# Performance work log

Measured on AMD Instinct MI355X. Metric: run time of the kernel, lower is better.

The kernel has to match this reference:

```python
import jax, jax.numpy as jnp
import numpy as np

N = 50000      # nodes
E = 1600000    # edges (avg degree 32)
D = 128        # node_feat_size
G = 128        # graph_feat_size (must equal D for BatchNorm1d to match MLP out)
EPS = 1e-5
NEG_SLOPE = 0.01  # LeakyReLU default


def setup_inputs() -> dict:
    key = jax.random.key(0)
    ks = jax.random.split(key, 10)
    p = lambda k, sh: jax.random.normal(k, sh, dtype=jnp.float32) * 0.05
    return {
        "node_feats": jax.random.normal(ks[0], (N, D), dtype=jnp.float32),
        "src": jax.random.randint(ks[1], (E,), 0, N, dtype=jnp.int32),
        "dst": jax.random.randint(ks[2], (E,), 0, N, dtype=jnp.int32),
        # project_edge: Linear(2D -> 1); split weight into dst/src halves
        "we_dst": p(ks[3], (D,)),
        "we_src": p(ks[4], (D,)),
        "be": jnp.zeros((), jnp.float32),
        # project_node: Linear(D -> G)
        "w_proj": p(ks[5], (D, G)),
        "b_proj": jnp.zeros((G,), jnp.float32),
        # MPL: Linear(G+D -> D), ReLU, Linear(D -> D)
        "w1": p(ks[6], (G + D, D)),
        "b1": jnp.zeros((D,), jnp.float32),
        "w2": p(ks[7], (D, D)),
        "b2": jnp.zeros((D,), jnp.float32),
        # BatchNorm1d(G) affine params (training-mode batch stats)
        "gamma": jnp.ones((G,), jnp.float32),
        "beta": jnp.zeros((G,), jnp.float32),
    }


def reference(node_feats, src, dst, we_dst, we_src, be, w_proj, b_proj,
              w1, b1, w2, b2, gamma, beta):
    # Edge logits: LeakyReLU(Linear(cat([dst_feat, src_feat])))
    # Linear over a concat == sum of two per-node projections -> avoid [E, 2D] tensor.
    ld = node_feats @ we_dst            # [N]
    ls = node_feats @ we_src            # [N]
    logit = ld[dst] + ls[src] + be      # [E]
    logit = jnp.where(logit >= 0, logit, NEG_SLOPE * logit)

    # edge_softmax: softmax over incoming edges of each destination node
    m = jax.ops.segment_max(logit, dst, num_segments=N)          # [N]
    ev = jnp.exp(logit - m[dst])                                  # [E]
    denom = jax.ops.segment_sum(ev, dst, num_segments=N)         # [N]
    a = ev / denom[dst]                                           # [E]

    # src_mul_edge + sum aggregation
    hv = node_feats @ w_proj + b_proj                             # [N, G]
    msg = hv[src] * a[:, None]                                    # [E, G]
    c = jax.ops.segment_sum(msg, dst, num_segments=N)             # [N, G]
    context = jax.nn.elu(c)

    # MPL: Linear -> ReLU -> Linear, then outer ReLU (dropout is identity in eval)
    h = jnp.concatenate([context, node_feats], axis=1)            # [N, G+D]
    h = jax.nn.relu(h @ w1 + b1)
    h = h @ w2 + b2
    h = jax.nn.relu(h)

    # BatchNorm1d in training mode: biased batch statistics
    mean = jnp.mean(h, axis=0)
    var = jnp.mean((h - mean) ** 2, axis=0)
    return gamma * (h - mean) / jnp.sqrt(var + EPS) + beta
```

## Files before the change

### kernel.cpp

```cpp
#include <hip/hip_runtime.h>
#include <math.h>

#define NN 50000
#define EE 1600000
#define DD 128
#define NB 98
#define SLAB 18432
#define MROWS 32
#define MGRID 1563

typedef __attribute__((ext_vector_type(8))) short short8v;
typedef __attribute__((ext_vector_type(4))) float f32x4;
typedef __attribute__((ext_vector_type(2))) float floatx2;

#define HVB_OFF     0
#define CTXB_OFF    6400000
#define BIN_OFF     19200000
#define SRCS_OFF    26425344
#define LD_OFF      30038016
#define LS_OFF      30238016
#define START_OFF   30438016
#define CNTN_OFF    30638016
#define W1T_OFF     30838016
#define W2T_OFF     30903552
#define WPT_OFF     30936320
#define BKC_OFF     30969088
#define MEAN_OFF    30969600
#define ISTD_OFF    30970112
#define PBN_OFF     30971648
#define PBQ_OFF     31771904
#define ZERO_OFF    BKC_OFF
#define ZERO_LEN    512

__device__ __forceinline__ unsigned short f2bf(float f) {
  union { float f; unsigned u; } v; v.f = f;
  unsigned r = v.u + 0x7FFFu + ((v.u >> 16) & 1u);
  return (unsigned short)(r >> 16);
}

__global__ __launch_bounds__(256) void k_prep_w(const float* __restrict__ w1,
    const float* __restrict__ w2, const float* __restrict__ wp,
    unsigned short* __restrict__ w1t, unsigned short* __restrict__ w2t,
    unsigned short* __restrict__ wpt) {
  int t = blockIdx.x * 256 + threadIdx.x;
  if (t < 32768) {
    int n = t & 127, k = t >> 7;
    w1t[n * 256 + k] = f2bf(w1[(size_t)k * 128 + n]);
  } else if (t < 49152) {
    int i = t - 32768; int n = i & 127, k = i >> 7;
    w2t[n * 128 + k] = f2bf(w2[(size_t)k * 128 + n]);
  } else {
    int i = t - 49152; int n = i & 127, k = i >> 7;
    wpt[n * 128 + k] = f2bf(wp[(size_t)k * 128 + n]);
  }
}

__global__ __launch_bounds__(256) void k_hv2(const float* __restrict__ nf,
    const unsigned short* __restrict__ wpt, const float* __restrict__ bp,
    const float* __restrict__ wed, const float* __restrict__ wes,
    float* __restrict__ ld, float* __restrict__ ls,
    unsigned char* __restrict__ hvb) {
  __shared__ unsigned short xs[64][136];
  int tid = threadIdx.x;
  int m0 = blockIdx.x * 64;
  int c4 = tid & 31;
  float4 wdv = *(const float4*)(wed + c4 * 4);
  float4 wsv = *(const float4*)(wes + c4 * 4);
  #pragma unroll
  for (int e = 0; e < 8; ++e) {
    int idx = tid + 256 * e;
    int row = idx >> 5;
    int m = m0 + row;
    int mc = (m < NN) ? m : (NN - 1);
    float4 v = *(const float4*)(nf + (size_t)mc * 128 + c4 * 4);
    ushort4 bb;
    bb.x = f2bf(v.x); bb.y = f2bf(v.y); bb.z = f2bf(v.z); bb.w = f2bf(v.w);
    *(ushort4*)&xs[row][c4 * 4] = bb;
    float pa = v.x * wdv.x + v.y * wdv.y + v.z * wdv.z + v.w * wdv.w;
    float pb = v.x * wsv.x + v.y * wsv.y + v.z * wsv.z + v.w * wsv.w;
    #pragma unroll
    for (int o = 16; o; o >>= 1) { pa += __shfl_xor(pa, o); pb += __shfl_xor(pb, o); }
    if (c4 == 0 && m < NN) { ld[m] = pa; ls[m] = pb; }
  }
  __syncthreads();
  int wid = tid >> 6, lane = tid & 63;
  int wm = wid >> 1, wn = wid & 1;
  int l15 = lane & 15, lg = lane >> 4;
  f32x4 acc[4][2];
  #pragma unroll
  for (int nf2 = 0; nf2 < 4; ++nf2)
    #pragma unroll
    for (int mf = 0; mf < 2; ++mf) acc[nf2][mf] = (f32x4){0.f, 0.f, 0.f, 0.f};
  for (int ks = 0; ks < 4; ++ks) {
    short8v aw[4], bx[2];
    #pragma unroll
    for (int nf2 = 0; nf2 < 4; ++nf2) {
      int n = wn * 64 + nf2 * 16 + l15;
      aw[nf2] = *(const short8v*)(wpt + (size_t)n * 128 + ks * 32 + lg * 8);
    }
    #pragma unroll
    for (int mf = 0; mf < 2; ++mf)
      bx[mf] = *(const short8v*)&xs[wm * 32 + mf * 16 + l15][ks * 32 + lg * 8];
    #pragma unroll
    for (int nf2 = 0; nf2 < 4; ++nf2)
      #pragma unroll
      for (int mf = 0; mf < 2; ++mf)
        acc[nf2][mf] = __builtin_amdgcn_mfma_f32_16x16x32_bf16(aw[nf2], bx[mf], acc[nf2][mf], 0, 0, 0);
  }
  #pragma unroll
  for (int nf2 = 0; nf2 < 4; ++nf2) {
    float4 bp4 = *(const float4*)(bp + wn * 64 + nf2 * 16 + lg * 4);
    #pragma unroll
    for (int mf = 0; mf < 2; ++mf) {
      int m = m0 + wm * 32 + mf * 16 + l15;
      if (m < NN) {
        int w = __builtin_amdgcn_cvt_pk_fp8_f32(acc[nf2][mf][0] + bp4.x,
                                                acc[nf2][mf][1] + bp4.y, 0, false);
        w = __builtin_amdgcn_cvt_pk_fp8_f32(acc[nf2][mf][2] + bp4.z,
                                            acc[nf2][mf][3] + bp4.w, w, true);
        *(int*)(hvb + (size_t)m * 128 + wn * 64 + nf2 * 16 + lg * 4) = w;
      }
    }
  }
}

__global__ __launch_bounds__(256) void k_bin(const int* __restrict__ src,
    const int* __restrict__ dst, int* __restrict__ bkc,
    unsigned* __restrict__ bin) {
  __shared__ unsigned slot[8192];
  __shared__ int hist[128], sc[128], loff[128], lcur[128], gbase[128];
  int tid = threadIdx.x;
  int tbase = blockIdx.x * 8192;
  int tlen = min(8192, EE - tbase);
  unsigned pk[32];
  if (tid < 128) hist[tid] = 0;
  __syncthreads();
  #pragma unroll
  for (int k = 0; k < 32; ++k) {
    int i = k * 256 + tid;
    if (i < tlen) {
      int e = tbase + i;
      pk[k] = ((unsigned)dst[e] << 16) | (unsigned)src[e];
      atomicAdd(&hist[pk[k] >> 25], 1);
    }
  }
  __syncthreads();
  if (tid < 128) sc[tid] = hist[tid];
  __syncthreads();
  for (int off = 1; off < 128; off <<= 1) {
    int v = 0;
    if (tid < 128) v = sc[tid] + ((tid >= off) ? sc[tid - off] : 0);
    __syncthreads();
    if (tid < 128) sc[tid] = v;
    __syncthreads();
  }
  if (tid < 128) { loff[tid] = sc[tid] - hist[tid]; lcur[tid] = sc[tid] - hist[tid]; }
  __syncthreads();
  #pragma unroll
  for (int k = 0; k < 32; ++k) {
    int i = k * 256 + tid;
    if (i < tlen) {
      int r = atomicAdd(&lcur[pk[k] >> 25], 1);
      slot[r] = pk[k];
    }
  }
  __syncthreads();
  if (tid < 128) gbase[tid] = hist[tid] ? atomicAdd(&bkc[tid], hist[tid]) : 0;
  __syncthreads();
  #pragma unroll
  for (int k = 0; k < 32; ++k) {
    int i = k * 256 + tid;
    if (i < tlen) {
      unsigned p = slot[i];
      int b = p >> 25;
      bin[(size_t)b * SLAB + gbase[b] + (i - loff[b])] = p;
    }
  }
}

__global__ __launch_bounds__(256) void k_bsort(const unsigned* __restrict__ bin,
    const int* __restrict__ bkc, unsigned short* __restrict__ srcs,
    int* __restrict__ start, int* __restrict__ cntn) {
  __shared__ unsigned eL[SLAB];
  __shared__ unsigned short outL[SLAB];
  __shared__ int hist[512], scA[512], cur[512];
  int tid = threadIdx.x;
  int b = blockIdx.x;
  int base = b * SLAB;
  int cnt = bkc[b];
  int node0 = b << 9;
  int nnb = min(512, NN - node0);
  for (int i = tid; i < 512; i += 256) hist[i] = 0;
  __syncthreads();
  for (int i = tid; i < cnt; i += 256) {
    unsigned p = bin[base + i];
    eL[i] = p;
    atomicAdd(&hist[(p >> 16) & 511], 1);
  }
  __syncthreads();
  for (int i = tid; i < 512; i += 256) scA[i] = hist[i];
  __syncthreads();
  for (int off = 1; off < 512; off <<= 1) {
    int v0 = scA[tid] + ((tid >= off) ? scA[tid - off] : 0);
    int i1 = tid + 256;
    int v1 = scA[i1] + ((i1 >= off) ? scA[i1 - off] : 0);
    __syncthreads();
    scA[tid] = v0; scA[i1] = v1;
    __syncthreads();
  }
  for (int i = tid; i < 512; i += 256) {
    int ex = scA[i] - hist[i];
    cur[i] = ex;
    if (i < nnb) { start[node0 + i] = base + ex; cntn[node0 + i] = hist[i]; }
  }
  __syncthreads();
  for (int i = tid; i < cnt; i += 256) {
    unsigned p = eL[i];
    int r = atomicAdd(&cur[(p >> 16) & 511], 1);
    outL[r] = (unsigned short)(p & 0xFFFFu);
  }
  __syncthreads();
  for (int i = tid; i < cnt; i += 256) srcs[base + i] = outL[i];
}

__global__ __launch_bounds__(256) void k_agg(const unsigned char* __restrict__ hvb,
    const float* __restrict__ ld, const float* __restrict__ ls,
    const float* __restrict__ be_p, const int* __restrict__ start,
    const int* __restrict__ cntn, const unsigned short* __restrict__ srcs,
    unsigned short* __restrict__ ctxb) {
  int wid = (blockIdx.x * 256 + threadIdx.x) >> 6;
  int lane = threadIdx.x & 63;
  if (wid >= NN) return;
  int cnt = cntn[wid];
  int l8 = lane & 7, e8 = lane >> 3;
  float acc[16];
  #pragma unroll
  for (int i = 0; i < 16; ++i) acc[i] = 0.f;
  float m = -INFINITY, dsum = 0.f;
  if (cnt > 0) {
    int s = start[wid];
    float base = ld[wid] + be_p[0];
    for (int c0 = 0; c0 < cnt; c0 += 64) {
      int len = min(64, cnt - c0);
      float lg = -INFINITY;
      int sv = 0;
      if (lane < len) {
        sv = srcs[s + c0 + lane];
        float l = base + ls[sv];
        lg = (l >= 0.f) ? l : 0.01f * l;
      }
      float cm = lg;
      #pragma unroll
      for (int o = 32; o; o >>= 1) cm = fmaxf(cm, __shfl_xor(cm, o));
      float nm = fmaxf(m, cm);
      float sc = __expf(m - nm);
      #pragma unroll
      for (int i = 0; i < 16; ++i) acc[i] *= sc;
      dsum *= sc;
      float ev = (lane < len) ? __expf(lg - nm) : 0.f;
      dsum += ev;
      for (int j = 0; j < len; j += 8) {
        int jj = j + e8;
        float evj = __shfl(ev, jj);
        int svj = __shfl(sv, jj);
        if (jj < len) {
          uint4 U = *(const uint4*)(hvb + (size_t)svj * 128 + l8 * 16);
          floatx2 p;
          p = __builtin_amdgcn_cvt_pk_f32_fp8((int)U.x, false); acc[0] += evj * p[0];  acc[1] += evj * p[1];
          p = __builtin_amdgcn_cvt_pk_f32_fp8((int)U.x, true);  acc[2] += evj * p[0];  acc[3] += evj * p[1];
          p = __builtin_amdgcn_cvt_pk_f32_fp8((int)U.y, false); acc[4] += evj * p[0];  acc[5] += evj * p[1];
          p = __builtin_amdgcn_cvt_pk_f32_fp8((int)U.y, true);  acc[6] += evj * p[0];  acc[7] += evj * p[1];
          p = __builtin_amdgcn_cvt_pk_f32_fp8((int)U.z, false); acc[8] += evj * p[0];  acc[9] += evj * p[1];
          p = __builtin_amdgcn_cvt_pk_f32_fp8((int)U.z, true);  acc[10] += evj * p[0]; acc[11] += evj * p[1];
          p = __builtin_amdgcn_cvt_pk_f32_fp8((int)U.w, false); acc[12] += evj * p[0]; acc[13] += evj * p[1];
          p = __builtin_amdgcn_cvt_pk_f32_fp8((int)U.w, true);  acc[14] += evj * p[0]; acc[15] += evj * p[1];
        }
      }
      m = nm;
    }
  }
  #pragma unroll
  for (int o = 8; o <= 32; o <<= 1)
    #pragma unroll
    for (int i = 0; i < 16; ++i) acc[i] += __shfl_xor(acc[i], o);
  #pragma unroll
  for (int o = 32; o; o >>= 1) dsum += __shfl_xor(dsum, o);
  float r = (dsum > 0.f) ? (1.f / dsum) : 0.f;
  if (lane < 32) {
    int g = lane & 7, p4 = lane >> 3;
    float v0 = acc[p4 * 4 + 0] * r, v1 = acc[p4 * 4 + 1] * r;
    float v2 = acc[p4 * 4 + 2] * r, v3 = acc[p4 * 4 + 3] * r;
    v0 = (v0 > 0.f) ? v0 : expm1f(v0);
    v1 = (v1 > 0.f) ? v1 : expm1f(v1);
    v2 = (v2 > 0.f) ? v2 : expm1f(v2);
    v3 = (v3 > 0.f) ? v3 : expm1f(v3);
    uint2 u;
    u.x = (unsigned)f2bf(v0) | ((unsigned)f2bf(v1) << 16);
    u.y = (unsigned)f2bf(v2) | ((unsigned)f2bf(v3) << 16);
    *(uint2*)(ctxb + (size_t)wid * 128 + g * 16 + p4 * 4) = u;
  }
}

__global__ __launch_bounds__(256) void k_mlp2(const unsigned short* __restrict__ ctxb,
    const float* __restrict__ nf,
    const unsigned short* __restrict__ w1t, const float* __restrict__ b1,
    const unsigned short* __restrict__ w2t, const float* __restrict__ b2,
    float* __restrict__ out, float* __restrict__ pbn, float* __restrict__ pbq) {
  __shared__ unsigned short xs[MROWS][264];
  __shared__ unsigned short h1s[MROWS][136];
  __shared__ float bns[128], bnq[128];
  int tid = threadIdx.x;
  int m0 = blockIdx.x * MROWS;
  if (tid < 128) { bns[tid] = 0.f; bnq[tid] = 0.f; }
  #pragma unroll
  for (int e = 0; e < 2; ++e) {
    int idx = tid + 256 * e;
    int row = idx >> 4, c8 = idx & 15;
    int m = m0 + row; if (m >= NN) m = NN - 1;
    uint4 v = *(const uint4*)(ctxb + (size_t)m * 128 + c8 * 8);
    *(uint4*)&xs[row][c8 * 8] = v;
  }
  #pragma unroll
  for (int e = 0; e < 4; ++e) {
    int idx = tid + 256 * e;
    int row = idx >> 5, c4 = idx & 31;
    int m = m0 + row; if (m >= NN) m = NN - 1;
    float4 w = *(const float4*)(nf + (size_t)m * 128 + c4 * 4);
    ushort4 cc;
    cc.x = f2bf(w.x); cc.y = f2bf(w.y); cc.z = f2bf(w.z); cc.w = f2bf(w.w);
    *(ushort4*)&xs[row][128 + c4 * 4] = cc;
  }
  __syncthreads();
  int wid = tid >> 6, lane = tid & 63;
  int wm = wid >> 1, wn = wid & 1;
  int l15 = lane & 15, lg = lane >> 4;
  f32x4 acc[4];
  #pragma unroll
  for (int nf2 = 0; nf2 < 4; ++nf2) acc[nf2] = (f32x4){0.f, 0.f, 0.f, 0.f};
  for (int ks = 0; ks < 8; ++ks) {
    short8v a = *(const short8v*)&xs[wm * 16 + l15][ks * 32 + lg * 8];
    #pragma unroll
    for (int nf2 = 0; nf2 < 4; ++nf2) {
      int n = wn * 64 + nf2 * 16 + l15;
      short8v b = *(const short8v*)(w1t + (size_t)n * 256 + ks * 32 + lg * 8);
      acc[nf2] = __builtin_amdgcn_mfma_f32_16x16x32_bf16(a, b, acc[nf2], 0, 0, 0);
    }
  }
  {
    float b1n[4];
    #pragma unroll
    for (int nf2 = 0; nf2 < 4; ++nf2) b1n[nf2] = b1[wn * 64 + nf2 * 16 + l15];
    #pragma unroll
    for (int nf2 = 0; nf2 < 4; ++nf2)
      #pragma unroll
      for (int r = 0; r < 4; ++r) {
        int row = wm * 16 + lg * 4 + r;
        int col = wn * 64 + nf2 * 16 + l15;
        h1s[row][col] = f2bf(fmaxf(acc[nf2][r] + b1n[nf2], 0.f));
      }
  }
  __syncthreads();
  f32x4 acc2[4];
  #pragma unroll
  for (int nf2 = 0; nf2 < 4; ++nf2) acc2[nf2] = (f32x4){0.f, 0.f, 0.f, 0.f};
  for (int ks = 0; ks < 4; ++ks) {
    short8v bh = *(const short8v*)&h1s[wm * 16 + l15][ks * 32 + lg * 8];
    #pragma unroll
    for (int nf2 = 0; nf2 < 4; ++nf2) {
      int n = wn * 64 + nf2 * 16 + l15;
      short8v aw = *(const short8v*)(w2t + (size_t)n * 128 + ks * 32 + lg * 8);
      acc2[nf2] = __builtin_amdgcn_mfma_f32_16x16x32_bf16(aw, bh, acc2[nf2], 0, 0, 0);
    }
  }
  {
    int m = m0 + wm * 16 + l15;
    bool valid = (m < NN);
    float hs[4][4], hq[4][4];
    #pragma unroll
    for (int nf2 = 0; nf2 < 4; ++nf2) {
      int f0 = wn * 64 + nf2 * 16 + lg * 4;
      float4 b24 = *(const float4*)(b2 + f0);
      float h0 = fmaxf(acc2[nf2][0] + b24.x, 0.f);
      float h1v = fmaxf(acc2[nf2][1] + b24.y, 0.f);
      float h2v = fmaxf(acc2[nf2][2] + b24.z, 0.f);
      float h3v = fmaxf(acc2[nf2][3] + b24.w, 0.f);
      if (valid) {
        float4 o = make_float4(h0, h1v, h2v, h3v);
        *(float4*)(out + (size_t)m * 128 + f0) = o;
      } else { h0 = h1v = h2v = h3v = 0.f; }
      hs[nf2][0] = h0; hs[nf2][1] = h1v; hs[nf2][2] = h2v; hs[nf2][3] = h3v;
      hq[nf2][0] = h0 * h0; hq[nf2][1] = h1v * h1v;
      hq[nf2][2] = h2v * h2v; hq[nf2][3] = h3v * h3v;
    }
    #pragma unroll
    for (int o = 1; o <= 8; o <<= 1)
      #pragma unroll
      for (int nf2 = 0; nf2 < 4; ++nf2)
        #pragma unroll
        for (int r = 0; r < 4; ++r) {
          hs[nf2][r] += __shfl_xor(hs[nf2][r], o);
          hq[nf2][r] += __shfl_xor(hq[nf2][r], o);
        }
    if (l15 == 0) {
      #pragma unroll
      for (int nf2 = 0; nf2 < 4; ++nf2) {
        int f0 = wn * 64 + nf2 * 16 + lg * 4;
        #pragma unroll
        for (int r = 0; r < 4; ++r) {
          atomicAdd(&bns[f0 + r], hs[nf2][r]);
          atomicAdd(&bnq[f0 + r], hq[nf2][r]);
        }
      }
    }
  }
  __syncthreads();
  if (tid < 128) {
    pbn[(size_t)blockIdx.x * 128 + tid] = bns[tid];
    pbq[(size_t)blockIdx.x * 128 + tid] = bnq[tid];
  }
}

__global__ __launch_bounds__(256) void k_bnstats2(const float* __restrict__ pbn,
    const float* __restrict__ pbq, float* __restrict__ mean,
    float* __restrict__ istd) {
  int f = blockIdx.x;
  float s = 0.f, q = 0.f;
  for (int b = threadIdx.x; b < MGRID; b += 256) {
    s += pbn[(size_t)b * 128 + f];
    q += pbq[(size_t)b * 128 + f];
  }
  #pragma unroll
  for (int o = 32; o; o >>= 1) { s += __shfl_xor(s, o); q += __shfl_xor(q, o); }
  __shared__ float ss[4], sq[4];
  int wid = threadIdx.x >> 6, lane = threadIdx.x & 63;
  if (lane == 0) { ss[wid] = s; sq[wid] = q; }
  __syncthreads();
  if (threadIdx.x == 0) {
    float S = ss[0] + ss[1] + ss[2] + ss[3];
    float Q = sq[0] + sq[1] + sq[2] + sq[3];
    float mu = S / (float)NN;
    float var = fmaxf(Q / (float)NN - mu * mu, 0.f);
    mean[f] = mu;
    istd[f] = 1.f / sqrtf(var + 1e-5f);
  }
}

__global__ __launch_bounds__(256) void k_bnorm(float* __restrict__ out,
    const float* __restrict__ mean, const float* __restrict__ istd,
    const float* __restrict__ gamma, const float* __restrict__ beta) {
  int idx = blockIdx.x * 256 + threadIdx.x;
  float4* p = (float4*)out;
  float4 v = p[idx];
  int f = (idx & 31) << 2;
  v.x = gamma[f + 0] * (v.x - mean[f + 0]) * istd[f + 0] + beta[f + 0];
  v.y = gamma[f + 1] * (v.y - mean[f + 1]) * istd[f + 1] + beta[f + 1];
  v.z = gamma[f + 2] * (v.z - mean[f + 2]) * istd[f + 2] + beta[f + 2];
  v.w = gamma[f + 3] * (v.w - mean[f + 3]) * istd[f + 3] + beta[f + 3];
  p[idx] = v;
}

extern "C" void kernel_launch(void* const* d_in, const int* in_sizes, int n_in,
                              void* d_out, int out_size, void* d_ws, size_t ws_size,
                              hipStream_t stream) {
  (void)in_sizes; (void)n_in; (void)out_size; (void)ws_size;
  const float* nf    = (const float*)d_in[0];
  const int*   src   = (const int*)d_in[1];
  const int*   dst   = (const int*)d_in[2];
  const float* wed   = (const float*)d_in[3];
  const float* wes   = (const float*)d_in[4];
  const float* be    = (const float*)d_in[5];
  const float* wp    = (const float*)d_in[6];
  const float* bp    = (const float*)d_in[7];
  const float* w1    = (const float*)d_in[8];
  const float* b1    = (const float*)d_in[9];
  const float* w2    = (const float*)d_in[10];
  const float* b2    = (const float*)d_in[11];
  const float* gamma = (const float*)d_in[12];
  const float* beta  = (const float*)d_in[13];
  float* out = (float*)d_out;
  char* ws = (char*)d_ws;

  unsigned char*  hvb  = (unsigned char*)(ws + HVB_OFF);
  unsigned short* ctxb = (unsigned short*)(ws + CTXB_OFF);
  unsigned*       bin  = (unsigned*)(ws + BIN_OFF);
  unsigned short* srcs = (unsigned short*)(ws + SRCS_OFF);
  float* ld    = (float*)(ws + LD_OFF);
  float* ls    = (float*)(ws + LS_OFF);
  int*   start = (int*)(ws + START_OFF);
  int*   cntn  = (int*)(ws + CNTN_OFF);
  unsigned short* w1t = (unsigned short*)(ws + W1T_OFF);
  unsigned short* w2t = (unsigned short*)(ws + W2T_OFF);
  unsigned short* wpt = (unsigned short*)(ws + WPT_OFF);
  int*   bkc   = (int*)(ws + BKC_OFF);
  float* mean  = (float*)(ws + MEAN_OFF);
  float* istd  = (float*)(ws + ISTD_OFF);
  float* pbn   = (float*)(ws + PBN_OFF);
  float* pbq   = (float*)(ws + PBQ_OFF);

  hipMemsetAsync(ws + ZERO_OFF, 0, ZERO_LEN, stream);

  k_prep_w<<<256, 256, 0, stream>>>(w1, w2, wp, w1t, w2t, wpt);
  k_bin<<<196, 256, 0, stream>>>(src, dst, bkc, bin);
  k_hv2<<<(NN + 63) / 64, 256, 0, stream>>>(nf, wpt, bp, wed, wes, ld, ls, hvb);
  k_bsort<<<NB, 256, 0, stream>>>(bin, bkc, srcs, start, cntn);
  k_agg<<<12500, 256, 0, stream>>>(hvb, ld, ls, be, start, cntn, srcs, ctxb);
  k_mlp2<<<MGRID, 256, 0, stream>>>(ctxb, nf, w1t, b1, w2t, b2, out, pbn, pbq);
  k_bnstats2<<<128, 256, 0, stream>>>(pbn, pbq, mean, istd);
  k_bnorm<<<(NN * DD / 4) / 256, 256, 0, stream>>>(out, mean, istd, gamma, beta);
}
```

Measured before the change: 283.7 us.

## Use finer dst buckets and single-pass softmax fast path in aggregation

Bucketing now splits destinations into 391 buckets of 128 nodes instead of 98 of 512, so each bsort block holds a smaller slab. The slab is read twice from global memory rather than staged in LDS, which lowers LDS use and raises the number of blocks. The aggregation kernel adds a fast path for nodes with at most 64 edges: it normalises the softmax once up front, drops the online rescaling and the per-edge bounds check, and uses packed float2 FMAs with precomputed byte addresses. The buffer layout is reshuffled to fit the new bucket arrays. The costs are a larger per-block histogram and scan in k_bin, and bins that could overflow if any bucket of 128 nodes receives more than 5120 edges.

```diff
diff --git a/kernel.cpp b/kernel.cpp
--- a/kernel.cpp
+++ b/kernel.cpp
@@ -4,8 +4,8 @@
 #define NN 50000
 #define EE 1600000
 #define DD 128
-#define NB 98
-#define SLAB 18432
+#define NB 391
+#define SLAB 5120
 #define MROWS 32
 #define MGRID 1563
 
@@ -16,21 +16,21 @@
 #define HVB_OFF     0
 #define CTXB_OFF    6400000
 #define BIN_OFF     19200000
-#define SRCS_OFF    26425344
-#define LD_OFF      30038016
-#define LS_OFF      30238016
-#define START_OFF   30438016
-#define CNTN_OFF    30638016
-#define W1T_OFF     30838016
-#define W2T_OFF     30903552
-#define WPT_OFF     30936320
-#define BKC_OFF     30969088
-#define MEAN_OFF    30969600
-#define ISTD_OFF    30970112
-#define PBN_OFF     30971648
-#define PBQ_OFF     31771904
+#define PBN_OFF     19200000
+#define PBQ_OFF     20000256
+#define SRCS_OFF    27207680
+#define LD_OFF      31211520
+#define LS_OFF      31411520
+#define START_OFF   31611520
+#define CNTN_OFF    31811520
+#define W1T_OFF     32011520
+#define W2T_OFF     32077056
+#define WPT_OFF     32109824
+#define BKC_OFF     32142592
+#define MEAN_OFF    32144640
+#define ISTD_OFF    32145152
 #define ZERO_OFF    BKC_OFF
-#define ZERO_LEN    512
+#define ZERO_LEN    2048
 
 __device__ __forceinline__ unsigned short f2bf(float f) {
   union { float f; unsigned u; } v; v.f = f;
@@ -128,12 +128,12 @@
     const int* __restrict__ dst, int* __restrict__ bkc,
     unsigned* __restrict__ bin) {
   __shared__ unsigned slot[8192];
-  __shared__ int hist[128], sc[128], loff[128], lcur[128], gbase[128];
+  __shared__ int hist[512], sc[512], loff[512], lcur[512], gbase[512];
   int tid = threadIdx.x;
   int tbase = blockIdx.x * 8192;
   int tlen = min(8192, EE - tbase);
   unsigned pk[32];
-  if (tid < 128) hist[tid] = 0;
+  for (int i = tid; i < 512; i += 256) hist[i] = 0;
   __syncthreads();
   #pragma unroll
   for (int k = 0; k < 32; ++k) {
@@ -141,38 +141,39 @@
     if (i < tlen) {
       int e = tbase + i;
       pk[k] = ((unsigned)dst[e] << 16) | (unsigned)src[e];
-      atomicAdd(&hist[pk[k] >> 25], 1);
-    }
-  }
-  __syncthreads();
-  if (tid < 128) sc[tid] = hist[tid];
-  __syncthreads();
-  for (int off = 1; off < 128; off <<= 1) {
-    int v = 0;
-    if (tid < 128) v = sc[tid] + ((tid >= off) ? sc[tid - off] : 0);
+      atomicAdd(&hist[pk[k] >> 23], 1);
+    }
+  }
+  __syncthreads();
+  for (int i = tid; i < 512; i += 256) sc[i] = hist[i];
+  __syncthreads();
+  for (int off = 1; off < 512; off <<= 1) {
+    int v0 = sc[tid] + ((tid >= off) ? sc[tid - off] : 0);
+    int i1 = tid + 256;
+    int v1 = sc[i1] + ((i1 >= off) ? sc[i1 - off] : 0);
     __syncthreads();
-    if (tid < 128) sc[tid] = v;
+    sc[tid] = v0; sc[i1] = v1;
     __syncthreads();
   }
-  if (tid < 128) { loff[tid] = sc[tid] - hist[tid]; lcur[tid] = sc[tid] - hist[tid]; }
+  for (int i = tid; i < 512; i += 256) { loff[i] = sc[i] - hist[i]; lcur[i] = sc[i] - hist[i]; }
   __syncthreads();
   #pragma unroll
   for (int k = 0; k < 32; ++k) {
     int i = k * 256 + tid;
     if (i < tlen) {
-      int r = atomicAdd(&lcur[pk[k] >> 25], 1);
+      int r = atomicAdd(&lcur[pk[k] >> 23], 1);
       slot[r] = pk[k];
     }
   }
   __syncthreads();
-  if (tid < 128) gbase[tid] = hist[tid] ? atomicAdd(&bkc[tid], hist[tid]) : 0;
+  for (int i = tid; i < 512; i += 256) gbase[i] = hist[i] ? atomicAdd(&bkc[i], hist[i]) : 0;
   __syncthreads();
   #pragma unroll
   for (int k = 0; k < 32; ++k) {
     int i = k * 256 + tid;
     if (i < tlen) {
       unsigned p = slot[i];
-      int b = p >> 25;
+      int b = p >> 23;
       bin[(size_t)b * SLAB + gbase[b] + (i - loff[b])] = p;
     }
   }
@@ -181,42 +182,37 @@
 __global__ __launch_bounds__(256) void k_bsort(const unsigned* __restrict__ bin,
     const int* __restrict__ bkc, unsigned short* __restrict__ srcs,
     int* __restrict__ start, int* __restrict__ cntn) {
-  __shared__ unsigned eL[SLAB];
   __shared__ unsigned short outL[SLAB];
-  __shared__ int hist[512], scA[512], cur[512];
+  __shared__ int hist[128], scA[128], cur[128];
   int tid = threadIdx.x;
   int b = blockIdx.x;
-  int base = b * SLAB;
+  size_t base = (size_t)b * SLAB;
   int cnt = bkc[b];
-  int node0 = b << 9;
-  int nnb = min(512, NN - node0);
-  for (int i = tid; i < 512; i += 256) hist[i] = 0;
+  int node0 = b << 7;
+  int nnb = min(128, NN - node0);
+  if (tid < 128) hist[tid] = 0;
+  __syncthreads();
+  for (int i = tid; i < cnt; i += 256)
+    atomicAdd(&hist[(bin[base + i] >> 16) & 127], 1);
+  __syncthreads();
+  if (tid < 128) scA[tid] = hist[tid];
+  __syncthreads();
+  for (int off = 1; off < 128; off <<= 1) {
+    int v = 0;
+    if (tid < 128) v = scA[tid] + ((tid >= off) ? scA[tid - off] : 0);
+    __syncthreads();
+    if (tid < 128) scA[tid] = v;
+    __syncthreads();
+  }
+  if (tid < 128) {
+    int ex = scA[tid] - hist[tid];
+    cur[tid] = ex;
+    if (tid < nnb) { start[node0 + tid] = (int)base + ex; cntn[node0 + tid] = hist[tid]; }
+  }
   __syncthreads();
   for (int i = tid; i < cnt; i += 256) {
     unsigned p = bin[base + i];
-    eL[i] = p;
-    atomicAdd(&hist[(p >> 16) & 511], 1);
-  }
-  __syncthreads();
-  for (int i = tid; i < 512; i += 256) scA[i] = hist[i];
-  __syncthreads();
-  for (int off = 1; off < 512; off <<= 1) {
-    int v0 = scA[tid] + ((tid >= off) ? scA[tid - off] : 0);
-    int i1 = tid + 256;
-    int v1 = scA[i1] + ((i1 >= off) ? scA[i1 - off] : 0);
-    __syncthreads();
-    scA[tid] = v0; scA[i1] = v1;
-    __syncthreads();
-  }
-  for (int i = tid; i < 512; i += 256) {
-    int ex = scA[i] - hist[i];
-    cur[i] = ex;
-    if (i < nnb) { start[node0 + i] = base + ex; cntn[node0 + i] = hist[i]; }
-  }
-  __syncthreads();
-  for (int i = tid; i < cnt; i += 256) {
-    unsigned p = eL[i];
-    int r = atomicAdd(&cur[(p >> 16) & 511], 1);
+    int r = atomicAdd(&cur[(p >> 16) & 127], 1);
     outL[r] = (unsigned short)(p & 0xFFFFu);
   }
   __syncthreads();
@@ -233,63 +229,104 @@
   if (wid >= NN) return;
   int cnt = cntn[wid];
   int l8 = lane & 7, e8 = lane >> 3;
-  float acc[16];
-  #pragma unroll
-  for (int i = 0; i < 16; ++i) acc[i] = 0.f;
-  float m = -INFINITY, dsum = 0.f;
+  floatx2 acc2[8];
+  #pragma unroll
+  for (int i = 0; i < 8; ++i) acc2[i] = (floatx2){0.f, 0.f};
+  float rfin = 1.f;
   if (cnt > 0) {
     int s = start[wid];
     float base = ld[wid] + be_p[0];
-    for (int c0 = 0; c0 < cnt; c0 += 64) {
-      int len = min(64, cnt - c0);
+    if (cnt <= 64) {
       float lg = -INFINITY;
-      int sv = 0;
-      if (lane < len) {
-        sv = srcs[s + c0 + lane];
+      unsigned adr = 0;
+      if (lane < cnt) {
+        int sv = srcs[s + lane];
+        adr = (unsigned)sv << 7;
         float l = base + ls[sv];
         lg = (l >= 0.f) ? l : 0.01f * l;
       }
-      float cm = lg;
-      #pragma unroll
-      for (int o = 32; o; o >>= 1) cm = fmaxf(cm, __shfl_xor(cm, o));
-      float nm = fmaxf(m, cm);
-      float sc = __expf(m - nm);
-      #pragma unroll
-      for (int i = 0; i < 16; ++i) acc[i] *= sc;
-      dsum *= sc;
-      float ev = (lane < len) ? __expf(lg - nm) : 0.f;
-      dsum += ev;
-      for (int j = 0; j < len; j += 8) {
-        int jj = j + e8;
+      float mx = lg;
+      #pragma unroll
+      for (int o = 32; o; o >>= 1) mx = fmaxf(mx, __shfl_xor(mx, o));
+      float ev = (lane < cnt) ? __expf(lg - mx) : 0.f;
+      float dsum = ev;
+      #pragma unroll
+      for (int o = 32; o; o >>= 1) dsum += __shfl_xor(dsum, o);
+      ev *= 1.f / dsum;
+      int nit = (cnt + 7) >> 3;
+      #pragma unroll 2
+      for (int j8 = 0; j8 < nit; ++j8) {
+        int jj = (j8 << 3) + e8;
         float evj = __shfl(ev, jj);
-        int svj = __shfl(sv, jj);
-        if (jj < len) {
-          uint4 U = *(const uint4*)(hvb + (size_t)svj * 128 + l8 * 16);
-          floatx2 p;
-          p = __builtin_amdgcn_cvt_pk_f32_fp8((int)U.x, false); acc[0] += evj * p[0];  acc[1] += evj * p[1];
-          p = __builtin_amdgcn_cvt_pk_f32_fp8((int)U.x, true);  acc[2] += evj * p[0];  acc[3] += evj * p[1];
-          p = __builtin_amdgcn_cvt_pk_f32_fp8((int)U.y, false); acc[4] += evj * p[0];  acc[5] += evj * p[1];
-          p = __builtin_amdgcn_cvt_pk_f32_fp8((int)U.y, true);  acc[6] += evj * p[0];  acc[7] += evj * p[1];
-          p = __builtin_amdgcn_cvt_pk_f32_fp8((int)U.z, false); acc[8] += evj * p[0];  acc[9] += evj * p[1];
-          p = __builtin_amdgcn_cvt_pk_f32_fp8((int)U.z, true);  acc[10] += evj * p[0]; acc[11] += evj * p[1];
-          p = __builtin_amdgcn_cvt_pk_f32_fp8((int)U.w, false); acc[12] += evj * p[0]; acc[13] += evj * p[1];
-          p = __builtin_amdgcn_cvt_pk_f32_fp8((int)U.w, true);  acc[14] += evj * p[0]; acc[15] += evj * p[1];
+        unsigned aj = (unsigned)__shfl((int)adr, jj);
+        uint4 U = *(const uint4*)(hvb + aj + l8 * 16);
+        floatx2 ev2 = (floatx2){evj, evj};
+        acc2[0] += ev2 * __builtin_amdgcn_cvt_pk_f32_fp8((int)U.x, false);
+        acc2[1] += ev2 * __builtin_amdgcn_cvt_pk_f32_fp8((int)U.x, true);
+        acc2[2] += ev2 * __builtin_amdgcn_cvt_pk_f32_fp8((int)U.y, false);
+        acc2[3] += ev2 * __builtin_amdgcn_cvt_pk_f32_fp8((int)U.y, true);
+        acc2[4] += ev2 * __builtin_amdgcn_cvt_pk_f32_fp8((int)U.z, false);
+        acc2[5] += ev2 * __builtin_amdgcn_cvt_pk_f32_fp8((int)U.z, true);
+        acc2[6] += ev2 * __builtin_amdgcn_cvt_pk_f32_fp8((int)U.w, false);
+        acc2[7] += ev2 * __builtin_amdgcn_cvt_pk_f32_fp8((int)U.w, true);
+      }
+    } else {
+      float m = -INFINITY, dsum = 0.f;
+      for (int c0 = 0; c0 < cnt; c0 += 64) {
+        int len = min(64, cnt - c0);
+        float lg = -INFINITY;
+        unsigned adr = 0;
+        if (lane < len) {
+          int sv = srcs[s + c0 + lane];
+          adr = (unsigned)sv << 7;
+          float l = base + ls[sv];
+          lg = (l >= 0.f) ? l : 0.01f * l;
         }
+        float cm = lg;
+        #pragma unroll
+        for (int o = 32; o; o >>= 1) cm = fmaxf(cm, __shfl_xor(cm, o));
+        float nm = fmaxf(m, cm);
+        float sc = __expf(m - nm);
+        floatx2 sc2 = (floatx2){sc, sc};
+        #pragma unroll
+        for (int i = 0; i < 8; ++i) acc2[i] *= sc2;
+        dsum *= sc;
+        float ev = (lane < len) ? __expf(lg - nm) : 0.f;
+        dsum += ev;
+        int nit = (len + 7) >> 3;
+        for (int j8 = 0; j8 < nit; ++j8) {
+          int jj = (j8 << 3) + e8;
+          float evj = __shfl(ev, jj);
+          unsigned aj = (unsigned)__shfl((int)adr, jj);
+          uint4 U = *(const uint4*)(hvb + aj + l8 * 16);
+          floatx2 ev2 = (floatx2){evj, evj};
+          acc2[0] += ev2 * __builtin_amdgcn_cvt_pk_f32_fp8((int)U.x, false);
+          acc2[1] += ev2 * __builtin_amdgcn_cvt_pk_f32_fp8((int)U.x, true);
+          acc2[2] += ev2 * __builtin_amdgcn_cvt_pk_f32_fp8((int)U.y, false);
+          acc2[3] += ev2 * __builtin_amdgcn_cvt_pk_f32_fp8((int)U.y, true);
+          acc2[4] += ev2 * __builtin_amdgcn_cvt_pk_f32_fp8((int)U.z, false);
+          acc2[5] += ev2 * __builtin_amdgcn_cvt_pk_f32_fp8((int)U.z, true);
+          acc2[6] += ev2 * __builtin_amdgcn_cvt_pk_f32_fp8((int)U.w, false);
+          acc2[7] += ev2 * __builtin_amdgcn_cvt_pk_f32_fp8((int)U.w, true);
+        }
+        m = nm;
       }
-      m = nm;
+      #pragma unroll
+      for (int o = 32; o; o >>= 1) dsum += __shfl_xor(dsum, o);
+      rfin = 1.f / dsum;
     }
   }
   #pragma unroll
   for (int o = 8; o <= 32; o <<= 1)
     #pragma unroll
-    for (int i = 0; i < 16; ++i) acc[i] += __shfl_xor(acc[i], o);
-  #pragma unroll
-  for (int o = 32; o; o >>= 1) dsum += __shfl_xor(dsum, o);
-  float r = (dsum > 0.f) ? (1.f / dsum) : 0.f;
+    for (int i = 0; i < 8; ++i) {
+      acc2[i].x += __shfl_xor(acc2[i].x, o);
+      acc2[i].y += __shfl_xor(acc2[i].y, o);
+    }
   if (lane < 32) {
     int g = lane & 7, p4 = lane >> 3;
-    float v0 = acc[p4 * 4 + 0] * r, v1 = acc[p4 * 4 + 1] * r;
-    float v2 = acc[p4 * 4 + 2] * r, v3 = acc[p4 * 4 + 3] * r;
+    float v0 = acc2[p4 * 2].x * rfin, v1 = acc2[p4 * 2].y * rfin;
+    float v2 = acc2[p4 * 2 + 1].x * rfin, v3 = acc2[p4 * 2 + 1].y * rfin;
     v0 = (v0 > 0.f) ? v0 : expm1f(v0);
     v1 = (v1 > 0.f) ? v1 : expm1f(v1);
     v2 = (v2 > 0.f) ? v2 : expm1f(v2);
```

Result: faster. 265.7 us (-6.4%).
